# Kernel optimization log

Hardware: AMD Instinct MI355X
Metric: run time of the kernel (lower is better)

The kernel has to match this reference:

```python
import jax, jax.numpy as jnp
import numpy as np

B, K, S, H, V, T = 32, 5, 64, 768, 30522, 40
SEP = 102


def setup_inputs() -> dict:
    key = jax.random.key(0)
    ks = jax.random.split(key, 8)
    s = 0.02
    return {
        "src": jax.random.normal(ks[0], (B, S, H), jnp.float32),
        "E": jax.random.normal(ks[1], (V, H), jnp.float32) * s,
        "Wa": jax.random.normal(ks[2], (H, H), jnp.float32) * s,
        "Ua": jax.random.normal(ks[3], (H, H), jnp.float32) * s,
        "va": jax.random.normal(ks[4], (H,), jnp.float32) * s,
        "W_ih": jax.random.normal(ks[5], (3 * H, 2 * H), jnp.float32) * s,
        "W_hh": jax.random.normal(ks[6], (3 * H, H), jnp.float32) * s,
        "b_ih": jnp.zeros((3 * H,), jnp.float32),
        "b_hh": jnp.zeros((3 * H,), jnp.float32),
        "Wo": jax.random.normal(ks[7], (V, H), jnp.float32) * s,
        "bo": jnp.zeros((V,), jnp.float32),
    }


def _decoder(tok, src, h, E, Wa, Ua, va, W_ih, W_hh, b_ih, b_hh, Wo, bo):
    # tok [N] int, src [N,S,H], h [N,H] -> (logits [N,V], h_new [N,H])
    emb = E[tok]                                              # [N,H]
    e = jnp.tanh(src @ Wa + (h @ Ua)[:, None, :]) @ va        # [N,S]
    a = jax.nn.softmax(e, axis=-1)
    ctx = jnp.einsum('ns,nsd->nd', a, src)                    # [N,H]
    x = jnp.concatenate([emb, ctx], axis=-1)                  # [N,2H]
    gx = x @ W_ih.T + b_ih
    gh = h @ W_hh.T + b_hh
    xr, xz, xn = jnp.split(gx, 3, axis=-1)
    hr, hz, hn = jnp.split(gh, 3, axis=-1)
    r = jax.nn.sigmoid(xr + hr)
    z = jax.nn.sigmoid(xz + hz)
    n = jnp.tanh(xn + r * hn)
    h2 = (1.0 - z) * n + z * h
    return h2 @ Wo.T + bo, h2


def _search(src, E, Wa, Ua, va, W_ih, W_hh, b_ih, b_hh, Wo, bo):
    P = (E, Wa, Ua, va, W_ih, W_hh, b_ih, b_hh, Wo, bo)
    # step 0: start token 102, zero hidden
    tok0 = jnp.full((B,), SEP, jnp.int32)
    logits, h = _decoder(tok0, src, jnp.zeros((B, H), src.dtype), *P)
    logp = jax.nn.log_softmax(logits, axis=-1)
    scores, toks = jax.lax.top_k(logp, K)                     # [B,K]
    hiddens = jnp.broadcast_to(h[:, None, :], (B, K, H))
    src_k = jnp.broadcast_to(src[:, None], (B, K, S, H)).reshape(B * K, S, H)
    no_prob = jnp.full((V,), -1e9, src.dtype).at[SEP].set(0.0)
    beam_mask = jnp.arange(K) < K - 1  # original normalizes only first k-1 segments

    def body(carry, _):
        toks, maps, hiddens, scores, ended, lengths = carry
        # parent hidden per beam (gather by backpointer), decode all beams at once
        h_in = jnp.take_along_axis(hiddens, maps[:, :, None], axis=1)  # [B,K,H]
        logits, h_new = _decoder(toks.reshape(-1), src_k, h_in.reshape(B * K, H), *P)
        logp = jax.nn.log_softmax(logits, axis=-1).reshape(B, K, V)
        logp = jnp.where(ended[:, :, None] == 0, logp, no_prob)
        lengths = lengths + (ended == 0).astype(lengths.dtype)
        cand = logp + scores[:, :, None]                      # [B,K,V]
        denom = jnp.where(beam_mask, lengths ** 0.7, 1.0)     # [B,K]
        norm = (cand / denom[:, :, None]).reshape(B, K * V)
        _, idx = jax.lax.top_k(norm, K)                       # [B,K]
        new_scores = jnp.take_along_axis(cand.reshape(B, K * V), idx, axis=1)
        new_toks = (idx % V).astype(jnp.int32)
        new_maps = (idx // V).astype(jnp.int32)
        ended = jnp.where(new_toks == SEP, 1.0, ended)
        new_carry = (new_toks, new_maps, h_new.reshape(B, K, H), new_scores, ended, lengths)
        return new_carry, (new_toks, new_maps)

    carry0 = (toks.astype(jnp.int32), jnp.zeros((B, K), jnp.int32), hiddens,
              scores, jnp.zeros((B, K), src.dtype), jnp.zeros((B, K), src.dtype))
    carryF, (toks_seq, maps_seq) = jax.lax.scan(body, carry0, None, length=T - 1)
    toks_all = jnp.concatenate([toks[None].astype(jnp.int32), toks_seq], axis=0)   # [T,B,K]
    maps_all = jnp.concatenate([jnp.zeros((1, B, K), jnp.int32), maps_seq], axis=0)
    final_scores = carryF[3]
    best = jnp.argmax(final_scores, axis=1).astype(jnp.int32)  # [B]

    def back(idx, tm):
        tk, mp = tm
        out = jnp.take_along_axis(tk, idx[:, None], axis=1)[:, 0]
        nxt = jnp.take_along_axis(mp, idx[:, None], axis=1)[:, 0]
        return nxt, out

    _, outs = jax.lax.scan(back, best, (toks_all, maps_all), reverse=True)
    return outs.T, final_scores  # tokens [B,T], scores [B,K]


def reference(src, E, Wa, Ua, va, W_ih, W_hh, b_ih, b_hh, Wo, bo):
    tokens, _ = _search(src, E, Wa, Ua, va, W_ih, W_hh, b_ih, b_hh, Wo, bo)
    return tokens
```

## Files before the change

kernel.cpp:

```cpp
#include <hip/hip_runtime.h>
#include <hip/hip_cooperative_groups.h>
#include <cmath>

namespace cg = cooperative_groups;

#define Hdim 768
#define Bb 32
#define Kb 5
#define Ss 64
#define Vv 30522
#define Tt 40
#define SEPTOK 102
#define NTLOG 477

typedef __attribute__((ext_vector_type(2))) float f32x2;
typedef __attribute__((ext_vector_type(4))) float f32x4;

struct Params {
    const float *src, *E, *Wa, *Ua, *va, *W_ih, *W_hh, *b_ih, *b_hh, *Wo, *bo;
    float *srcWa, *hA, *hB, *h_tmp, *h_g, *hUa, *xbuf, *gxE, *gx, *gh, *logits;
    float *maxpart, *mx, *lgs, *scores, *ended, *lengths;
    int *toks_cur, *maps_cur, *toks_all, *maps_all, *outTok;
};

__device__ __forceinline__ bool betterf(float va, int ja, float vb, int jb) {
    return (va > vb) || (va == vb && ja < jb);
}
__device__ __forceinline__ void ins5(float* tv, int* tj, float v, int j) {
    if (!betterf(v, j, tv[4], tj[4])) return;
    tv[4] = v; tj[4] = j;
#pragma unroll
    for (int q = 4; q > 0; q--) {
        if (betterf(tv[q], tj[q], tv[q - 1], tj[q - 1])) {
            float t = tv[q]; tv[q] = tv[q - 1]; tv[q - 1] = t;
            int  ti = tj[q]; tj[q] = tj[q - 1]; tj[q - 1] = ti;
        }
    }
}

union SMem {
    struct { float xs[32][162]; float wt[32][66]; } g;
    struct { float hu[Hdim]; float va[Hdim]; float e[Ss]; float a[Ss];
             float ctx[Hdim]; float gx[2304]; } at;
    struct { float sc[Kb], den[Kb], end[Kb], len[Kb], mxs[Kb], lgv[Kb];
             float mv[512 * 5]; int mj[512 * 5];
             float rv[512]; int rj[512]; double rd[512]; int selj[Kb]; } tk;
};

__device__ void gemm512(SMem& sm, const Params& P, int t, int N, int xsrc,
    int i0, int Pdim, const float* __restrict__ W, int ldW, bool pmaj,
    const float* __restrict__ bias, float* __restrict__ outp, int ldO,
    int Icap, float* __restrict__ maxpart, int tileIdx)
{
    const int tid = threadIdx.x;
    const int ty = tid >> 5, tx = tid & 31;
    const float* h_old = (t & 1) ? P.hB : P.hA;
    const float* h_new = (t & 1) ? P.hA : P.hB;

    float acc[10][2];
#pragma unroll
    for (int j = 0; j < 10; j++) { acc[j][0] = 0.f; acc[j][1] = 0.f; }

    for (int c0 = 0; c0 < Pdim; c0 += 32) {
        __syncthreads();
        for (int e = tid; e < 160 * 32; e += 512) {
            int r = e >> 5, p = e & 31;
            int n = (r < N) ? r : (N - 1);
            float v = 0.f;
            if (xsrc == 0) {
                if (t != 0) {
                    int par = (n / Kb) * Kb + P.maps_cur[n];
                    v = h_old[(size_t)par * Hdim + c0 + p];
                }
            } else if (xsrc == 1) {
                int tok = (t == 0) ? SEPTOK : P.toks_cur[n];
                v = P.E[(size_t)tok * Hdim + c0 + p];
            } else {
                int rowMul = (t == 0) ? Kb : 1;
                v = h_new[((size_t)n * rowMul) * Hdim + c0 + p];
            }
            sm.g.xs[p][r] = v;
        }
        if (pmaj) {
            int p = tid >> 4, i4 = (tid & 15) * 4;
            int gi = i0 + i4;
            f32x4 a;
            if (gi + 3 < Icap) {
                a = *(const f32x4*)&W[(size_t)(c0 + p) * ldW + gi];
            } else {
#pragma unroll
                for (int u = 0; u < 4; u++) {
                    int g = gi + u; if (g >= Icap) g = Icap - 1;
                    a[u] = W[(size_t)(c0 + p) * ldW + g];
                }
            }
            *(f32x4*)&sm.g.wt[p][i4] = a;
        } else {
            int c = tid >> 3, p4 = (tid & 7) * 4;
            int gi = i0 + c; if (gi >= Icap) gi = Icap - 1;
            f32x4 a = *(const f32x4*)&W[(size_t)gi * ldW + c0 + p4];
            sm.g.wt[p4 + 0][c] = a[0]; sm.g.wt[p4 + 1][c] = a[1];
            sm.g.wt[p4 + 2][c] = a[2]; sm.g.wt[p4 + 3][c] = a[3];
        }
        __syncthreads();
        float part[10][2];
#pragma unroll
        for (int j = 0; j < 10; j++) { part[j][0] = 0.f; part[j][1] = 0.f; }
#pragma unroll
        for (int p = 0; p < 32; p++) {
            f32x2 w2 = *(const f32x2*)&sm.g.wt[p][tx * 2];
            float xr[10];
#pragma unroll
            for (int j = 0; j < 10; j += 2) {
                f32x2 xv = *(const f32x2*)&sm.g.xs[p][ty * 10 + j];
                xr[j] = xv.x; xr[j + 1] = xv.y;
            }
#pragma unroll
            for (int j = 0; j < 10; j++) {
                part[j][0] = fmaf(xr[j], w2.x, part[j][0]);
                part[j][1] = fmaf(xr[j], w2.y, part[j][1]);
            }
        }
#pragma unroll
        for (int j = 0; j < 10; j++) {
            acc[j][0] = __fadd_rn(acc[j][0], part[j][0]);
            acc[j][1] = __fadd_rn(acc[j][1], part[j][1]);
        }
    }
    float rmax[10];
#pragma unroll
    for (int j = 0; j < 10; j++) rmax[j] = -INFINITY;
#pragma unroll
    for (int j = 0; j < 10; j++) {
        int r = ty * 10 + j;
        if (r < N) {
#pragma unroll
            for (int u = 0; u < 2; u++) {
                int gi = i0 + tx * 2 + u;
                if (gi < Icap) {
                    float v = acc[j][u];
                    if (bias) v = __fadd_rn(v, bias[gi]);
                    outp[(size_t)r * ldO + gi] = v;
                    rmax[j] = fmaxf(rmax[j], v);
                }
            }
        }
    }
    if (maxpart) {
#pragma unroll
        for (int j = 0; j < 10; j++) {
#pragma unroll
            for (int off = 16; off; off >>= 1)
                rmax[j] = fmaxf(rmax[j], __shfl_xor(rmax[j], off, 32));
        }
        if (tx == 0) {
#pragma unroll
            for (int j = 0; j < 10; j++) {
                int r = ty * 10 + j;
                if (r < N) maxpart[(size_t)tileIdx * 160 + r] = rmax[j];
            }
        }
    }
}

__global__ __launch_bounds__(512) void step_k(Params P)
{
    cg::grid_group grid = cg::this_grid();
    __shared__ SMem sm;
    const int tid = threadIdx.x;
    const int gdim = gridDim.x;

    for (int t = 0; t < Tt; t++) {
        const int N = (t == 0) ? Bb : Bb * Kb;
        const int Kcur = (t == 0) ? 1 : Kb;
        float* h_new = (t & 1) ? P.hA : P.hB;
        const float* h_old = (t & 1) ? P.hB : P.hA;

        for (int task = blockIdx.x; task < 84; task += gdim) {
            if (task < 12)
                gemm512(sm, P, t, N, 0, task * 64, Hdim, P.Ua, Hdim, true,
                        nullptr, P.hUa, Hdim, Hdim, nullptr, 0);
            else if (task < 48)
                gemm512(sm, P, t, N, 0, (task - 12) * 64, Hdim, P.W_hh, Hdim, false,
                        P.b_hh, P.gh, 2304, 2304, nullptr, 0);
            else
                gemm512(sm, P, t, N, 1, (task - 48) * 64, Hdim, P.W_ih, 1536, false,
                        nullptr, P.gxE, 2304, 2304, nullptr, 0);
        }
        grid.sync();

        for (int n = blockIdx.x; n < N; n += gdim) {
            int b = n / Kcur;
            for (int j = tid; j < Hdim; j += 512) {
                sm.at.hu[j] = P.hUa[(size_t)n * Hdim + j];
                sm.at.va[j] = P.va[j];
            }
            __syncthreads();
            {
                int wv = tid >> 6, ln = tid & 63;
                for (int s = wv * 8; s < wv * 8 + 8; s++) {
                    const float* sw = P.srcWa + (size_t)(b * Ss + s) * Hdim;
                    double p = 0.0;
                    for (int j = ln; j < Hdim; j += 64) {
                        float tv = (float)tanh((double)__fadd_rn(sw[j], sm.at.hu[j]));
                        p = ::fma((double)tv, (double)sm.at.va[j], p);
                    }
                    for (int off = 32; off; off >>= 1) p += __shfl_down(p, off, 64);
                    if (ln == 0) sm.at.e[s] = (float)p;
                }
            }
            __syncthreads();
            if (tid < 64) {
                float v = sm.at.e[tid], m = v;
                for (int off = 32; off; off >>= 1) m = fmaxf(m, __shfl_xor(m, off, 64));
                float p = (float)exp((double)__fsub_rn(v, m));
                double sum = (double)p;
                for (int off = 32; off; off >>= 1) sum += __shfl_xor(sum, off, 64);
                sm.at.a[tid] = __fdiv_rn(p, (float)sum);
            }
            __syncthreads();
            for (int j = tid; j < Hdim; j += 512) {
                double acc = 0.0;
                for (int s = 0; s < Ss; s++)
                    acc = ::fma((double)sm.at.a[s],
                                (double)P.src[(size_t)(b * Ss + s) * Hdim + j], acc);
                sm.at.ctx[j] = (float)acc;
            }
            __syncthreads();
            for (int i = tid; i < 2304; i += 512) {
                const float* wr = P.W_ih + (size_t)i * 1536 + 768;
                float accv = 0.f, part = 0.f;
                for (int p = 0; p < 768; p += 4) {
                    f32x4 w4 = *(const f32x4*)&wr[p];
                    part = fmaf(sm.at.ctx[p + 0], w4[0], part);
                    part = fmaf(sm.at.ctx[p + 1], w4[1], part);
                    part = fmaf(sm.at.ctx[p + 2], w4[2], part);
                    part = fmaf(sm.at.ctx[p + 3], w4[3], part);
                    if ((p & 31) == 28) { accv = __fadd_rn(accv, part); part = 0.f; }
                }
                sm.at.gx[i] = __fadd_rn(__fadd_rn(P.gxE[(size_t)n * 2304 + i], accv),
                                        P.b_ih[i]);
            }
            __syncthreads();
            int par = 0;
            if (t != 0) par = (n / Kb) * Kb + P.maps_cur[n];
            for (int i = tid; i < Hdim; i += 512) {
                float xr = sm.at.gx[i], xz = sm.at.gx[768 + i], xn = sm.at.gx[1536 + i];
                const float* ghr = P.gh + (size_t)n * 2304;
                float hr = ghr[i], hz = ghr[768 + i], hn = ghr[1536 + i];
                float r  = (float)(1.0 / (1.0 + exp(-(double)__fadd_rn(xr, hr))));
                float z  = (float)(1.0 / (1.0 + exp(-(double)__fadd_rn(xz, hz))));
                float nn = (float)tanh((double)__fadd_rn(xn, __fmul_rn(r, hn)));
                float hv = (t == 0) ? 0.f : h_old[(size_t)par * Hdim + i];
                float h2 = __fadd_rn(__fmul_rn(__fsub_rn(1.f, z), nn), __fmul_rn(z, hv));
                if (t == 0) {
                    for (int k = 0; k < Kb; k++)
                        h_new[(size_t)(n * Kb + k) * Hdim + i] = h2;
                } else {
                    h_new[(size_t)n * Hdim + i] = h2;
                }
            }
            __syncthreads();
        }
        grid.sync();

        for (int task = blockIdx.x; task < NTLOG; task += gdim) {
            gemm512(sm, P, t, N, 2, task * 64, Hdim, P.Wo, Hdim, false,
                    P.bo, P.logits, Vv, Vv, P.maxpart, task);
        }
        grid.sync();

        for (int b = blockIdx.x; b < Bb; b += gdim) {
            if (tid < Kb) {
                if (t == 0) {
                    sm.tk.sc[tid] = 0.f; sm.tk.end[tid] = 0.f; sm.tk.len[tid] = 0.f;
                    sm.tk.den[tid] = 1.f;
                } else {
                    float e0 = P.ended[b * Kb + tid];
                    float ln = __fadd_rn(P.lengths[b * Kb + tid], (e0 == 0.f) ? 1.f : 0.f);
                    sm.tk.sc[tid]  = P.scores[b * Kb + tid];
                    sm.tk.end[tid] = e0;
                    sm.tk.len[tid] = ln;
                    sm.tk.den[tid] = (tid < Kb - 1) ? (float)pow((double)ln, (double)0.7f) : 1.f;
                }
            }
            __syncthreads();
            for (int k = 0; k < Kcur; k++) {
                bool active = (t == 0) || (sm.tk.end[k] == 0.f);
                if (!active) {
                    if (tid == 0) { sm.tk.mxs[k] = 0.f; sm.tk.lgv[k] = 0.f; }
                    __syncthreads();
                    continue;
                }
                int n = b * Kcur + k;
                float m = -INFINITY;
                for (int tile = tid; tile < NTLOG; tile += 512)
                    m = fmaxf(m, P.maxpart[(size_t)tile * 160 + n]);
                sm.tk.rv[tid] = m; __syncthreads();
                for (int off = 256; off; off >>= 1) {
                    if (tid < off) sm.tk.rv[tid] = fmaxf(sm.tk.rv[tid], sm.tk.rv[tid + off]);
                    __syncthreads();
                }
                m = sm.tk.rv[0];
                const float* lg = P.logits + (size_t)n * Vv;
                double s = 0.0;
                for (int v = tid; v < Vv; v += 512) {
                    float ex = (float)exp((double)__fsub_rn(lg[v], m));
                    s += (double)ex;
                }
                __syncthreads();
                sm.tk.rd[tid] = s; __syncthreads();
                for (int off = 256; off; off >>= 1) {
                    if (tid < off) sm.tk.rd[tid] += sm.tk.rd[tid + off];
                    __syncthreads();
                }
                if (tid == 0) {
                    sm.tk.mxs[k] = m;
                    float sf = (float)sm.tk.rd[0];
                    sm.tk.lgv[k] = (float)log((double)sf);
                }
                __syncthreads();
            }
            const float* lbase = P.logits + (size_t)b * Kcur * Vv;
            float tv[5]; int tj[5];
#pragma unroll
            for (int q = 0; q < 5; q++) { tv[q] = -INFINITY; tj[q] = 0x7fffffff; }
            for (int k = 0; k < Kcur; k++) {
                if (t == 0 || sm.tk.end[k] == 0.f) {
                    float m = sm.tk.mxs[k], l = sm.tk.lgv[k];
                    float sck = sm.tk.sc[k], den = sm.tk.den[k];
                    const float* lg = lbase + (size_t)k * Vv;
                    for (int v = tid; v < Vv; v += 512) {
                        float lp  = __fsub_rn(__fsub_rn(lg[v], m), l);
                        float val = __fdiv_rn(__fadd_rn(lp, sck), den);
                        ins5(tv, tj, val, k * Vv + v);
                    }
                } else if (tid == 0) {
                    float val = __fdiv_rn(sm.tk.sc[k], sm.tk.den[k]);
                    ins5(tv, tj, val, k * Vv + SEPTOK);
                }
            }
#pragma unroll
            for (int q = 0; q < 5; q++) { sm.tk.mv[tid * 5 + q] = tv[q]; sm.tk.mj[tid * 5 + q] = tj[q]; }
            __syncthreads();
            for (int pass = 0; pass < Kb; pass++) {
                float bv = -INFINITY; int bj = 0x7fffffff;
#pragma unroll
                for (int q = 0; q < 5; q++) {
                    float v = sm.tk.mv[tid * 5 + q]; int j = sm.tk.mj[tid * 5 + q];
                    if (betterf(v, j, bv, bj)) { bv = v; bj = j; }
                }
                sm.tk.rv[tid] = bv; sm.tk.rj[tid] = bj;
                __syncthreads();
                for (int off = 256; off; off >>= 1) {
                    if (tid < off) {
                        float ov = sm.tk.rv[tid + off]; int oj = sm.tk.rj[tid + off];
                        if (betterf(ov, oj, sm.tk.rv[tid], sm.tk.rj[tid])) {
                            sm.tk.rv[tid] = ov; sm.tk.rj[tid] = oj;
                        }
                    }
                    __syncthreads();
                }
                if (tid == 0) sm.tk.selj[pass] = sm.tk.rj[0];
                __syncthreads();
#pragma unroll
                for (int q = 0; q < 5; q++)
                    if (sm.tk.mj[tid * 5 + q] == sm.tk.selj[pass]) {
                        sm.tk.mv[tid * 5 + q] = -INFINITY; sm.tk.mj[tid * 5 + q] = 0x7fffffff;
                    }
                __syncthreads();
            }
            if (tid == 0) {
                for (int q = 0; q < Kb; q++) {
                    int jj = sm.tk.selj[q];
                    int pk = jj / Vv, vv = jj - pk * Vv;
                    float lp;
                    if (t == 0 || sm.tk.end[pk] == 0.f)
                        lp = __fsub_rn(__fsub_rn(lbase[(size_t)pk * Vv + vv], sm.tk.mxs[pk]),
                                       sm.tk.lgv[pk]);
                    else
                        lp = (vv == SEPTOK) ? 0.f : -1e9f;
                    float cand = __fadd_rn(lp, sm.tk.sc[pk]);
                    P.scores[b * Kb + q]   = cand;
                    P.toks_cur[b * Kb + q] = vv;
                    P.maps_cur[b * Kb + q] = (t == 0) ? 0 : pk;
                    if (t == 0) {
                        P.ended[b * Kb + q]   = 0.f;
                        P.lengths[b * Kb + q] = 0.f;
                    } else {
                        P.ended[b * Kb + q]   = (vv == SEPTOK) ? 1.f : sm.tk.end[q];
                        P.lengths[b * Kb + q] = sm.tk.len[q];
                    }
                    P.toks_all[(size_t)t * Bb * Kb + b * Kb + q] = vv;
                    P.maps_all[(size_t)t * Bb * Kb + b * Kb + q] = (t == 0) ? 0 : pk;
                }
            }
            __syncthreads();
        }
        grid.sync();
    }

    if (blockIdx.x == 0 && tid < Bb) {
        int b = tid;
        int best = 0; float bvv = P.scores[b * Kb];
        for (int k = 1; k < Kb; k++) {
            float v = P.scores[b * Kb + k];
            if (v > bvv) { bvv = v; best = k; }
        }
        int cur = best;
        for (int t = Tt - 1; t >= 0; t--) {
            P.outTok[b * Tt + t] = P.toks_all[t * Bb * Kb + b * Kb + cur];
            cur = P.maps_all[t * Bb * Kb + b * Kb + cur];
        }
    }
}

template<int RPT, int CPT, bool PMAJ>
__global__ __launch_bounds__(512) void gemmN_k(int P, int I, int xrs, int ldW,
    const float* __restrict__ X, const float* __restrict__ W,
    const float* __restrict__ bias, float* __restrict__ out, int ldO)
{
    constexpr int ROWS = RPT * 16;
    constexpr int COLS = CPT * 32;
    constexpr int XST  = ROWS + 4;
    constexpr int WST  = COLS + 4;
    __shared__ float xs[32][XST];
    __shared__ float wt[32][WST];
    const int tid = threadIdx.x;
    const int ty = tid >> 5, tx = tid & 31;
    const int row0 = blockIdx.y * ROWS;
    const int i0 = blockIdx.x * COLS;

    float acc[RPT][CPT];
#pragma unroll
    for (int j = 0; j < RPT; j++)
#pragma unroll
        for (int u = 0; u < CPT; u++) acc[j][u] = 0.f;

    for (int c0 = 0; c0 < P; c0 += 32) {
        __syncthreads();
        for (int e = tid; e < ROWS * 32; e += 512) {
            int r = e >> 5, p = e & 31;
            xs[p][r] = X[(size_t)(row0 + r) * xrs + c0 + p];
        }
        if (PMAJ) {
            for (int v = tid; v < 32 * (COLS / 4); v += 512) {
                int p  = v / (COLS / 4);
                int i4 = (v % (COLS / 4)) * 4;
                f32x4 a;
                if (i0 + i4 + 3 < I) {
                    a = *(const f32x4*)&W[(size_t)(c0 + p) * ldW + i0 + i4];
                } else {
#pragma unroll
                    for (int u = 0; u < 4; u++) {
                        int g = i0 + i4 + u; if (g >= I) g = I - 1;
                        a[u] = W[(size_t)(c0 + p) * ldW + g];
                    }
                }
                *(f32x4*)&wt[p][i4] = a;
            }
        } else {
            for (int v = tid; v < COLS * 8; v += 512) {
                int c  = v >> 3;
                int p4 = (v & 7) * 4;
                int gi = i0 + c; if (gi >= I) gi = I - 1;
                f32x4 a = *(const f32x4*)&W[(size_t)gi * ldW + c0 + p4];
                wt[p4 + 0][c] = a[0]; wt[p4 + 1][c] = a[1];
                wt[p4 + 2][c] = a[2]; wt[p4 + 3][c] = a[3];
            }
        }
        __syncthreads();
        float part[RPT][CPT];
#pragma unroll
        for (int j = 0; j < RPT; j++)
#pragma unroll
            for (int u = 0; u < CPT; u++) part[j][u] = 0.f;
#pragma unroll
        for (int p = 0; p < 32; p++) {
            float xr[RPT];
#pragma unroll
            for (int j = 0; j < RPT; j += 2) {
                f32x2 xv = *(const f32x2*)&xs[p][ty * RPT + j];
                xr[j] = xv.x; xr[j + 1] = xv.y;
            }
            float wv[CPT];
#pragma unroll
            for (int u = 0; u < CPT; u += 2) {
                f32x2 w2 = *(const f32x2*)&wt[p][tx * CPT + u];
                wv[u] = w2.x; wv[u + 1] = w2.y;
            }
#pragma unroll
            for (int j = 0; j < RPT; j++)
#pragma unroll
                for (int u = 0; u < CPT; u++)
                    part[j][u] = fmaf(xr[j], wv[u], part[j][u]);
        }
#pragma unroll
        for (int j = 0; j < RPT; j++)
#pragma unroll
            for (int u = 0; u < CPT; u++)
                acc[j][u] = __fadd_rn(acc[j][u], part[j][u]);
    }
#pragma unroll
    for (int j = 0; j < RPT; j++) {
        int gr = row0 + ty * RPT + j;
#pragma unroll
        for (int u = 0; u < CPT; u++) {
            int gi = i0 + tx * CPT + u;
            if (gi < I) {
                float v = acc[j][u];
                if (bias) v = __fadd_rn(v, bias[gi]);
                out[(size_t)gr * ldO + gi] = v;
            }
        }
    }
}

__global__ __launch_bounds__(256) void gather_k(int N, int Kcur,
    const int* __restrict__ maps, const int* __restrict__ toks,
    const float* __restrict__ h_beam, const float* __restrict__ E,
    float* __restrict__ h_g, float* __restrict__ xbuf)
{
    int n = blockIdx.x;
    if (n >= N) return;
    int b = n / Kcur;
    int tok = toks ? toks[n] : SEPTOK;
    const float* er = E + (size_t)tok * Hdim;
    if (maps) {
        const float* hs = h_beam + (size_t)(b * Kb + maps[n]) * Hdim;
        for (int j = threadIdx.x; j < Hdim; j += 256) {
            h_g[(size_t)n * Hdim + j]  = hs[j];
            xbuf[(size_t)n * 1536 + j] = er[j];
        }
    } else {
        for (int j = threadIdx.x; j < Hdim; j += 256) {
            h_g[(size_t)n * Hdim + j]  = 0.f;
            xbuf[(size_t)n * 1536 + j] = er[j];
        }
    }
}

__global__ __launch_bounds__(256) void bcast_k(const float* __restrict__ h_tmp,
                                               float* __restrict__ h_beam)
{
    int b = blockIdx.x;
    for (int j = threadIdx.x; j < Hdim; j += 256) {
        float v = h_tmp[(size_t)b * Hdim + j];
        for (int k = 0; k < Kb; k++)
            h_beam[(size_t)(b * Kb + k) * Hdim + j] = v;
    }
}

__global__ __launch_bounds__(256) void attn2_k(int N, int Kcur,
    const float* __restrict__ hUa, const float* __restrict__ srcWa,
    const float* __restrict__ src, const float* __restrict__ va,
    float* __restrict__ xbuf)
{
    __shared__ float hu[Hdim];
    __shared__ float va_s[Hdim];
    __shared__ float e_s[Ss];
    __shared__ float a_s[Ss];
    int n = blockIdx.x, tid = threadIdx.x;
    if (n >= N) return;
    int b = n / Kcur;
    for (int j = tid; j < Hdim; j += 256) {
        hu[j]   = hUa[(size_t)n * Hdim + j];
        va_s[j] = va[j];
    }
    __syncthreads();
    int wv = tid >> 6, ln = tid & 63;
    for (int s = wv * 16; s < wv * 16 + 16; s++) {
        const float* sw = srcWa + (size_t)(b * Ss + s) * Hdim;
        double p = 0.0;
        for (int j = ln; j < Hdim; j += 64) {
            float tv = (float)tanh((double)__fadd_rn(sw[j], hu[j]));
            p = ::fma((double)tv, (double)va_s[j], p);
        }
        for (int off = 32; off; off >>= 1) p += __shfl_down(p, off, 64);
        if (ln == 0) e_s[s] = (float)p;
    }
    __syncthreads();
    if (tid < 64) {
        float v = e_s[tid], m = v;
        for (int off = 32; off; off >>= 1) m = fmaxf(m, __shfl_xor(m, off, 64));
        float p = (float)exp((double)__fsub_rn(v, m));
        double sum = (double)p;
        for (int off = 32; off; off >>= 1) sum += __shfl_xor(sum, off, 64);
        a_s[tid] = __fdiv_rn(p, (float)sum);
    }
    __syncthreads();
    for (int j = tid; j < Hdim; j += 256) {
        double acc = 0.0;
        for (int s = 0; s < Ss; s++)
            acc = ::fma((double)a_s[s], (double)src[(size_t)(b * Ss + s) * Hdim + j], acc);
        xbuf[(size_t)n * 1536 + 768 + j] = (float)acc;
    }
}

__global__ __launch_bounds__(256) void gate_k(int N,
    const float* __restrict__ gx, const float* __restrict__ gh,
    const float* __restrict__ h_g, float* __restrict__ h_out)
{
    int idx = blockIdx.x * 256 + threadIdx.x;
    if (idx >= N * Hdim) return;
    int n = idx / Hdim, i = idx - n * Hdim;
    const float* gxr = gx + (size_t)n * 2304;
    const float* ghr = gh + (size_t)n * 2304;
    float xr = gxr[i], xz = gxr[768 + i], xn = gxr[1536 + i];
    float hr = ghr[i], hz = ghr[768 + i], hn = ghr[1536 + i];
    float r  = (float)(1.0 / (1.0 + exp(-(double)__fadd_rn(xr, hr))));
    float z  = (float)(1.0 / (1.0 + exp(-(double)__fadd_rn(xz, hz))));
    float nn = (float)tanh((double)__fadd_rn(xn, __fmul_rn(r, hn)));
    float hv = h_g[(size_t)n * Hdim + i];
    float h2 = __fadd_rn(__fmul_rn(__fsub_rn(1.f, z), nn), __fmul_rn(z, hv));
    h_out[(size_t)n * Hdim + i] = h2;
}

__global__ __launch_bounds__(256) void lse_k(int N,
    const float* __restrict__ logits, float* __restrict__ mx, float* __restrict__ lgs)
{
    __shared__ float  redf[256];
    __shared__ double redd[256];
    int n = blockIdx.x, tid = threadIdx.x;
    const float* lg = logits + (size_t)n * Vv;
    float m = -INFINITY;
    for (int v = tid; v < Vv; v += 256) m = fmaxf(m, lg[v]);
    redf[tid] = m; __syncthreads();
    for (int off = 128; off; off >>= 1) {
        if (tid < off) redf[tid] = fmaxf(redf[tid], redf[tid + off]);
        __syncthreads();
    }
    m = redf[0];
    double s = 0.0;
    for (int v = tid; v < Vv; v += 256) {
        float ex = (float)exp((double)__fsub_rn(lg[v], m));
        s += (double)ex;
    }
    redd[tid] = s; __syncthreads();
    for (int off = 128; off; off >>= 1) {
        if (tid < off) redd[tid] += redd[tid + off];
        __syncthreads();
    }
    if (tid == 0) {
        mx[n] = m;
        float sf = (float)redd[0];
        lgs[n] = (float)log((double)sf);
    }
}

__global__ __launch_bounds__(256) void topk5_k(int t,
    const float* __restrict__ logits, const float* __restrict__ mx, const float* __restrict__ lgs,
    float* scores, float* ended, float* lengths,
    int* toks_cur, int* maps_cur, int* toks_all, int* maps_all)
{
    __shared__ float sc_s[Kb], den_s[Kb], end_s[Kb], len_s[Kb], mx_s[Kb], lg_s[Kb];
    __shared__ float mv[256 * 5];
    __shared__ int   mj[256 * 5];
    __shared__ float rv[256];
    __shared__ int   rj[256];
    __shared__ int   selj[Kb];
    int b = blockIdx.x, tid = threadIdx.x;
    int Kcur = (t == 0) ? 1 : Kb;
    if (tid < Kb) {
        if (t == 0) {
            sc_s[tid] = 0.f; end_s[tid] = 0.f; len_s[tid] = 0.f; den_s[tid] = 1.f;
            mx_s[tid] = mx[b]; lg_s[tid] = lgs[b];
        } else {
            float e0 = ended[b * Kb + tid];
            float ln = __fadd_rn(lengths[b * Kb + tid], (e0 == 0.f) ? 1.f : 0.f);
            sc_s[tid]  = scores[b * Kb + tid];
            end_s[tid] = e0;
            len_s[tid] = ln;
            den_s[tid] = (tid < Kb - 1) ? (float)pow((double)ln, (double)0.7f) : 1.f;
            mx_s[tid]  = mx[b * Kb + tid];
            lg_s[tid]  = lgs[b * Kb + tid];
        }
    }
    __syncthreads();
    const float* lbase = logits + (size_t)b * Kcur * Vv;
    float tv[5]; int tj[5];
#pragma unroll
    for (int q = 0; q < 5; q++) { tv[q] = -INFINITY; tj[q] = 0x7fffffff; }
    for (int k = 0; k < Kcur; k++) {
        if (end_s[k] == 0.f) {
            float m = mx_s[k], l = lg_s[k], sck = sc_s[k], den = den_s[k];
            const float* lg = lbase + (size_t)k * Vv;
            for (int v = tid; v < Vv; v += 256) {
                float lp  = __fsub_rn(__fsub_rn(lg[v], m), l);
                float val = __fdiv_rn(__fadd_rn(lp, sck), den);
                ins5(tv, tj, val, k * Vv + v);
            }
        } else if (tid == 0) {
            float val = __fdiv_rn(sc_s[k], den_s[k]);
            ins5(tv, tj, val, k * Vv + SEPTOK);
        }
    }
#pragma unroll
    for (int q = 0; q < 5; q++) { mv[tid * 5 + q] = tv[q]; mj[tid * 5 + q] = tj[q]; }
    __syncthreads();
    for (int pass = 0; pass < Kb; pass++) {
        float bv = -INFINITY; int bj = 0x7fffffff;
#pragma unroll
        for (int q = 0; q < 5; q++) {
            float v = mv[tid * 5 + q]; int j = mj[tid * 5 + q];
            if (betterf(v, j, bv, bj)) { bv = v; bj = j; }
        }
        rv[tid] = bv; rj[tid] = bj;
        __syncthreads();
        for (int off = 128; off; off >>= 1) {
            if (tid < off) {
                float ov = rv[tid + off]; int oj = rj[tid + off];
                if (betterf(ov, oj, rv[tid], rj[tid])) { rv[tid] = ov; rj[tid] = oj; }
            }
            __syncthreads();
        }
        if (tid == 0) selj[pass] = rj[0];
        __syncthreads();
#pragma unroll
        for (int q = 0; q < 5; q++)
            if (mj[tid * 5 + q] == selj[pass]) { mv[tid * 5 + q] = -INFINITY; mj[tid * 5 + q] = 0x7fffffff; }
        __syncthreads();
    }
    if (tid == 0) {
        for (int q = 0; q < Kb; q++) {
            int jj = selj[q];
            int pk = jj / Vv, vv = jj - pk * Vv;
            float lp;
            if (end_s[pk] == 0.f)
                lp = __fsub_rn(__fsub_rn(lbase[(size_t)pk * Vv + vv], mx_s[pk]), lg_s[pk]);
            else
                lp = (vv == SEPTOK) ? 0.f : -1e9f;
            float cand = __fadd_rn(lp, sc_s[pk]);
            scores[b * Kb + q]   = cand;
            toks_cur[b * Kb + q] = vv;
            maps_cur[b * Kb + q] = (t == 0) ? 0 : pk;
            if (t == 0) {
                ended[b * Kb + q]   = 0.f;
                lengths[b * Kb + q] = 0.f;
            } else {
                ended[b * Kb + q]   = (vv == SEPTOK) ? 1.f : end_s[q];
                lengths[b * Kb + q] = len_s[q];
            }
            toks_all[(size_t)t * Bb * Kb + b * Kb + q] = vv;
            maps_all[(size_t)t * Bb * Kb + b * Kb + q] = (t == 0) ? 0 : pk;
        }
    }
}

__global__ void back_k(const float* __restrict__ scores,
                       const int* __restrict__ toks_all, const int* __restrict__ maps_all,
                       int* __restrict__ out)
{
    int b = threadIdx.x;
    if (b >= Bb) return;
    int best = 0; float bvv = scores[b * Kb];
    for (int k = 1; k < Kb; k++) {
        float v = scores[b * Kb + k];
        if (v > bvv) { bvv = v; best = k; }
    }
    int cur = best;
    for (int t = Tt - 1; t >= 0; t--) {
        out[b * Tt + t] = toks_all[t * Bb * Kb + b * Kb + cur];
        cur = maps_all[t * Bb * Kb + b * Kb + cur];
    }
}

extern "C" void kernel_launch(void* const* d_in, const int* in_sizes, int n_in,
                              void* d_out, int out_size, void* d_ws, size_t ws_size,
                              hipStream_t stream)
{
    Params P;
    P.src  = (const float*)d_in[0];
    P.E    = (const float*)d_in[1];
    P.Wa   = (const float*)d_in[2];
    P.Ua   = (const float*)d_in[3];
    P.va   = (const float*)d_in[4];
    P.W_ih = (const float*)d_in[5];
    P.W_hh = (const float*)d_in[6];
    P.b_ih = (const float*)d_in[7];
    P.b_hh = (const float*)d_in[8];
    P.Wo   = (const float*)d_in[9];
    P.bo   = (const float*)d_in[10];
    P.outTok = (int*)d_out;

    char* w = (char*)d_ws;
    size_t used = 0;
    auto alloc = [&](size_t bytes) -> char* {
        char* p = w + used;
        used += (bytes + 255) & ~(size_t)255;
        return p;
    };
    P.srcWa   = (float*)alloc((size_t)Bb * Ss * Hdim * 4);
    P.hA      = (float*)alloc((size_t)Bb * Kb * Hdim * 4);
    P.hB      = (float*)alloc((size_t)Bb * Kb * Hdim * 4);
    P.h_tmp   = (float*)alloc((size_t)Bb * Hdim * 4);
    P.h_g     = (float*)alloc((size_t)Bb * Kb * Hdim * 4);
    P.hUa     = (float*)alloc((size_t)Bb * Kb * Hdim * 4);
    P.xbuf    = (float*)alloc((size_t)Bb * Kb * 1536 * 4);
    P.gxE     = (float*)alloc((size_t)Bb * Kb * 2304 * 4);
    P.gx      = (float*)alloc((size_t)Bb * Kb * 2304 * 4);
    P.gh      = (float*)alloc((size_t)Bb * Kb * 2304 * 4);
    P.logits  = (float*)alloc((size_t)Bb * Kb * Vv * 4);
    P.maxpart = (float*)alloc((size_t)NTLOG * 160 * 4);
    P.mx      = (float*)alloc(Bb * Kb * 4);
    P.lgs     = (float*)alloc(Bb * Kb * 4);
    P.scores  = (float*)alloc(Bb * Kb * 4);
    P.ended   = (float*)alloc(Bb * Kb * 4);
    P.lengths = (float*)alloc(Bb * Kb * 4);
    P.toks_cur = (int*)alloc(Bb * Kb * 4);
    P.maps_cur = (int*)alloc(Bb * Kb * 4);
    P.toks_all = (int*)alloc((size_t)Tt * Bb * Kb * 4);
    P.maps_all = (int*)alloc((size_t)Tt * Bb * Kb * 4);

    gemmN_k<8, 2, true><<<dim3(12, 16), 512, 0, stream>>>(
        Hdim, Hdim, Hdim, Hdim, P.src, P.Wa, nullptr, P.srcWa, Hdim);

    int dev = 0;
    (void)hipGetDevice(&dev);
    int nCU = 256;
    (void)hipDeviceGetAttribute(&nCU, hipDeviceAttributeMultiprocessorCount, dev);
    int maxAct = 0;
    if (hipOccupancyMaxActiveBlocksPerMultiprocessor(&maxAct, step_k, 512, 0)
            != hipSuccess || maxAct < 1)
        maxAct = 1;
    long long gridLL = (long long)maxAct * (long long)nCU;
    if (gridLL > 256) gridLL = 256;
    if (gridLL < 1) gridLL = 1;
    dim3 grid((unsigned)gridLL);

    void* args[] = { (void*)&P };
    hipError_t err = hipLaunchCooperativeKernel((void*)step_k, grid, dim3(512),
                                                args, 0, stream);
    if (err != hipSuccess) {
        (void)hipGetLastError();
        for (int t = 0; t < Tt; t++) {
            int N  = (t == 0) ? Bb : Bb * Kb;
            int Kc = (t == 0) ? 1 : Kb;
            const int* mp = (t == 0) ? nullptr : P.maps_cur;
            const int* tk = (t == 0) ? nullptr : P.toks_cur;
            float* h_beam = P.hA;
            float* h_cur = (t == 0) ? P.h_tmp : h_beam;

            gather_k<<<N, 256, 0, stream>>>(N, Kc, mp, tk, h_beam, P.E, P.h_g, P.xbuf);
            if (t == 0) {
                gemmN_k<2, 2, true><<<dim3(12, 1), 512, 0, stream>>>(
                    Hdim, Hdim, Hdim, Hdim, P.h_g, P.Ua, nullptr, P.hUa, Hdim);
            } else {
                gemmN_k<10, 2, true><<<dim3(12, 1), 512, 0, stream>>>(
                    Hdim, Hdim, Hdim, Hdim, P.h_g, P.Ua, nullptr, P.hUa, Hdim);
            }
            attn2_k<<<N, 256, 0, stream>>>(N, Kc, P.hUa, P.srcWa, P.src, P.va, P.xbuf);
            if (t == 0) {
                gemmN_k<2, 2, false><<<dim3(36, 1), 512, 0, stream>>>(
                    1536, 2304, 1536, 1536, P.xbuf, P.W_ih, P.b_ih, P.gx, 2304);
                gemmN_k<2, 2, false><<<dim3(36, 1), 512, 0, stream>>>(
                    Hdim, 2304, Hdim, Hdim, P.h_g, P.W_hh, P.b_hh, P.gh, 2304);
            } else {
                gemmN_k<10, 2, false><<<dim3(36, 1), 512, 0, stream>>>(
                    1536, 2304, 1536, 1536, P.xbuf, P.W_ih, P.b_ih, P.gx, 2304);
                gemmN_k<10, 2, false><<<dim3(36, 1), 512, 0, stream>>>(
                    Hdim, 2304, Hdim, Hdim, P.h_g, P.W_hh, P.b_hh, P.gh, 2304);
            }
            gate_k<<<(N * Hdim + 255) / 256, 256, 0, stream>>>(N, P.gx, P.gh, P.h_g, h_cur);
            if (t == 0)
                bcast_k<<<Bb, 256, 0, stream>>>(P.h_tmp, h_beam);
            if (t == 0) {
                gemmN_k<2, 4, false><<<dim3(239, 1), 512, 0, stream>>>(
                    Hdim, Vv, Hdim, Hdim, h_cur, P.Wo, P.bo, P.logits, Vv);
            } else {
                gemmN_k<10, 4, false><<<dim3(239, 1), 512, 0, stream>>>(
                    Hdim, Vv, Hdim, Hdim, h_cur, P.Wo, P.bo, P.logits, Vv);
            }
            lse_k<<<N, 256, 0, stream>>>(N, P.logits, P.mx, P.lgs);
            topk5_k<<<Bb, 256, 0, stream>>>(t, P.logits, P.mx, P.lgs, P.scores,
                                            P.ended, P.lengths, P.toks_cur, P.maps_cur,
                                            P.toks_all, P.maps_all);
        }
        back_k<<<1, 64, 0, stream>>>(P.scores, P.toks_all, P.maps_all, P.outTok);
    }
}
```

Measured before the change: 46.17 ms.

## Fuse per-tile softmax stats and top-5 into logits GEMM epilogue

The logits GEMM now computes per-tile row max, a sum of exponentials, and a per-row top-5 in its epilogue, so the full logits matrix no longer has to be written and re-read. The top-k phase then merges the per-tile statistics instead of scanning all 30522 logits per beam. It also swaps double-precision tanh/exp in attention and the GRU for float intrinsics, pads the Wo tile layout, and raises the cooperative grid cap to 512 blocks. The float math may change numerics and tie behaviour relative to the double path, and the larger grid makes each grid sync more expensive.

```diff
diff --git a/kernel.cpp b/kernel.cpp
--- a/kernel.cpp
+++ b/kernel.cpp
@@ -19,7 +19,8 @@
 struct Params {
     const float *src, *E, *Wa, *Ua, *va, *W_ih, *W_hh, *b_ih, *b_hh, *Wo, *bo;
     float *srcWa, *hA, *hB, *h_tmp, *h_g, *hUa, *xbuf, *gxE, *gx, *gh, *logits;
-    float *maxpart, *mx, *lgs, *scores, *ended, *lengths;
+    float *mt_g; double *st_g; float *t5v; int *t5j;
+    float *mx, *lgs, *scores, *ended, *lengths;
     int *toks_cur, *maps_cur, *toks_all, *maps_all, *outTok;
 };
 
@@ -37,25 +38,37 @@
         }
     }
 }
+__device__ __forceinline__ void ins5p(float* tv, int* tj, float* tx,
+                                      float v, int j, float x) {
+    if (!betterf(v, j, tv[4], tj[4])) return;
+    tv[4] = v; tj[4] = j; tx[4] = x;
+#pragma unroll
+    for (int q = 4; q > 0; q--) {
+        if (betterf(tv[q], tj[q], tv[q - 1], tj[q - 1])) {
+            float t = tv[q]; tv[q] = tv[q - 1]; tv[q - 1] = t;
+            int  ti = tj[q]; tj[q] = tj[q - 1]; tj[q - 1] = ti;
+            float tz = tx[q]; tx[q] = tx[q - 1]; tx[q - 1] = tz;
+        }
+    }
+}
 
 union SMem {
-    struct { float xs[32][162]; float wt[32][66]; } g;
+    struct { float xs[32][162]; float wt[32][68]; } g;
     struct { float hu[Hdim]; float va[Hdim]; float e[Ss]; float a[Ss];
              float ctx[Hdim]; float gx[2304]; } at;
     struct { float sc[Kb], den[Kb], end[Kb], len[Kb], mxs[Kb], lgv[Kb];
-             float mv[512 * 5]; int mj[512 * 5];
-             float rv[512]; int rj[512]; double rd[512]; int selj[Kb]; } tk;
+             float mv[256 * 5]; int mj[256 * 5]; float mxp[256 * 5];
+             float rv[512]; int rj[512]; float rx[512]; double rd[512];
+             int selj[Kb]; float selx[Kb]; } tk;
 };
 
 __device__ void gemm512(SMem& sm, const Params& P, int t, int N, int xsrc,
     int i0, int Pdim, const float* __restrict__ W, int ldW, bool pmaj,
-    const float* __restrict__ bias, float* __restrict__ outp, int ldO,
-    int Icap, float* __restrict__ maxpart, int tileIdx)
+    const float* __restrict__ bias, float* __restrict__ outp, int ldO, int Icap)
 {
     const int tid = threadIdx.x;
     const int ty = tid >> 5, tx = tid & 31;
     const float* h_old = (t & 1) ? P.hB : P.hA;
-    const float* h_new = (t & 1) ? P.hA : P.hB;
 
     float acc[10][2];
 #pragma unroll
@@ -72,12 +85,9 @@
                     int par = (n / Kb) * Kb + P.maps_cur[n];
                     v = h_old[(size_t)par * Hdim + c0 + p];
                 }
-            } else if (xsrc == 1) {
+            } else {
                 int tok = (t == 0) ? SEPTOK : P.toks_cur[n];
                 v = P.E[(size_t)tok * Hdim + c0 + p];
-            } else {
-                int rowMul = (t == 0) ? Kb : 1;
-                v = h_new[((size_t)n * rowMul) * Hdim + c0 + p];
             }
             sm.g.xs[p][r] = v;
         }
@@ -127,9 +137,6 @@
             acc[j][1] = __fadd_rn(acc[j][1], part[j][1]);
         }
     }
-    float rmax[10];
-#pragma unroll
-    for (int j = 0; j < 10; j++) rmax[j] = -INFINITY;
 #pragma unroll
     for (int j = 0; j < 10; j++) {
         int r = ty * 10 + j;
@@ -141,23 +148,100 @@
                     float v = acc[j][u];
                     if (bias) v = __fadd_rn(v, bias[gi]);
                     outp[(size_t)r * ldO + gi] = v;
-                    rmax[j] = fmaxf(rmax[j], v);
-                }
-            }
-        }
-    }
-    if (maxpart) {
+                }
+            }
+        }
+    }
+}
+
+__device__ void logits_tile(SMem& sm, const Params& P, int t, int N, int task)
+{
+    const int tid = threadIdx.x;
+    const int ty = tid >> 5, tx = tid & 31;
+    const int i0 = task * 64;
+    const float* h_new = (t & 1) ? P.hA : P.hB;
+    const int rowMul = (t == 0) ? Kb : 1;
+
+    float acc[10][2];
+#pragma unroll
+    for (int j = 0; j < 10; j++) { acc[j][0] = 0.f; acc[j][1] = 0.f; }
+
+    for (int c0 = 0; c0 < Hdim; c0 += 32) {
+        __syncthreads();
+        for (int e = tid; e < 160 * 32; e += 512) {
+            int r = e >> 5, p = e & 31;
+            int n = (r < N) ? r : (N - 1);
+            sm.g.xs[p][r] = h_new[((size_t)n * rowMul) * Hdim + c0 + p];
+        }
+        {
+            int c = tid >> 3, p4 = (tid & 7) * 4;
+            int gi = i0 + c; if (gi >= Vv) gi = Vv - 1;
+            f32x4 a = *(const f32x4*)&P.Wo[(size_t)gi * Hdim + c0 + p4];
+            sm.g.wt[p4 + 0][c] = a[0]; sm.g.wt[p4 + 1][c] = a[1];
+            sm.g.wt[p4 + 2][c] = a[2]; sm.g.wt[p4 + 3][c] = a[3];
+        }
+        __syncthreads();
+        float part[10][2];
+#pragma unroll
+        for (int j = 0; j < 10; j++) { part[j][0] = 0.f; part[j][1] = 0.f; }
+#pragma unroll
+        for (int p = 0; p < 32; p++) {
+            f32x2 w2 = *(const f32x2*)&sm.g.wt[p][tx * 2];
+            float xr[10];
+#pragma unroll
+            for (int j = 0; j < 10; j += 2) {
+                f32x2 xv = *(const f32x2*)&sm.g.xs[p][ty * 10 + j];
+                xr[j] = xv.x; xr[j + 1] = xv.y;
+            }
+#pragma unroll
+            for (int j = 0; j < 10; j++) {
+                part[j][0] = fmaf(xr[j], w2.x, part[j][0]);
+                part[j][1] = fmaf(xr[j], w2.y, part[j][1]);
+            }
+        }
 #pragma unroll
         for (int j = 0; j < 10; j++) {
-#pragma unroll
-            for (int off = 16; off; off >>= 1)
-                rmax[j] = fmaxf(rmax[j], __shfl_xor(rmax[j], off, 32));
-        }
-        if (tx == 0) {
-#pragma unroll
-            for (int j = 0; j < 10; j++) {
-                int r = ty * 10 + j;
-                if (r < N) maxpart[(size_t)tileIdx * 160 + r] = rmax[j];
+            acc[j][0] = __fadd_rn(acc[j][0], part[j][0]);
+            acc[j][1] = __fadd_rn(acc[j][1], part[j][1]);
+        }
+    }
+#pragma unroll
+    for (int j = 0; j < 10; j++) {
+        int r = ty * 10 + j;
+        int g0 = i0 + tx * 2, g1 = g0 + 1;
+        float x0 = (g0 < Vv) ? __fadd_rn(acc[j][0], P.bo[g0]) : -INFINITY;
+        float x1 = (g1 < Vv) ? __fadd_rn(acc[j][1], P.bo[g1]) : -INFINITY;
+        float mr = fmaxf(x0, x1);
+#pragma unroll
+        for (int off = 16; off; off >>= 1)
+            mr = fmaxf(mr, __shfl_xor(mr, off, 32));
+        double s = (double)expf(__fsub_rn(x0, mr)) + (double)expf(__fsub_rn(x1, mr));
+#pragma unroll
+        for (int off = 16; off; off >>= 1)
+            s += __shfl_xor(s, off, 32);
+        float tv[5]; int tj[5];
+#pragma unroll
+        for (int q = 0; q < 5; q++) { tv[q] = -INFINITY; tj[q] = 0x7fffffff; }
+        ins5(tv, tj, x0, (g0 < Vv) ? g0 : 0x7fffffff);
+        ins5(tv, tj, x1, (g1 < Vv) ? g1 : 0x7fffffff);
+#pragma unroll
+        for (int lv = 1; lv < 32; lv <<= 1) {
+            float pv[5]; int pj[5];
+#pragma unroll
+            for (int q = 0; q < 5; q++) {
+                pv[q] = __shfl_xor(tv[q], lv, 32);
+                pj[q] = __shfl_xor(tj[q], lv, 32);
+            }
+#pragma unroll
+            for (int q = 0; q < 5; q++) ins5(tv, tj, pv[q], pj[q]);
+        }
+        if (tx == 0 && r < N) {
+            P.mt_g[(size_t)task * 160 + r] = mr;
+            P.st_g[(size_t)task * 160 + r] = s;
+#pragma unroll
+            for (int q = 0; q < 5; q++) {
+                P.t5v[((size_t)task * 160 + r) * 5 + q] = tv[q];
+                P.t5j[((size_t)task * 160 + r) * 5 + q] = tj[q];
             }
         }
     }
@@ -179,13 +263,13 @@
         for (int task = blockIdx.x; task < 84; task += gdim) {
             if (task < 12)
                 gemm512(sm, P, t, N, 0, task * 64, Hdim, P.Ua, Hdim, true,
-                        nullptr, P.hUa, Hdim, Hdim, nullptr, 0);
+                        nullptr, P.hUa, Hdim, Hdim);
             else if (task < 48)
                 gemm512(sm, P, t, N, 0, (task - 12) * 64, Hdim, P.W_hh, Hdim, false,
-                        P.b_hh, P.gh, 2304, 2304, nullptr, 0);
+                        P.b_hh, P.gh, 2304, 2304);
             else
                 gemm512(sm, P, t, N, 1, (task - 48) * 64, Hdim, P.W_ih, 1536, false,
-                        nullptr, P.gxE, 2304, 2304, nullptr, 0);
+                        nullptr, P.gxE, 2304, 2304);
         }
         grid.sync();
 
@@ -202,7 +286,7 @@
                     const float* sw = P.srcWa + (size_t)(b * Ss + s) * Hdim;
                     double p = 0.0;
                     for (int j = ln; j < Hdim; j += 64) {
-                        float tv = (float)tanh((double)__fadd_rn(sw[j], sm.at.hu[j]));
+                        float tv = tanhf(__fadd_rn(sw[j], sm.at.hu[j]));
                         p = ::fma((double)tv, (double)sm.at.va[j], p);
                     }
                     for (int off = 32; off; off >>= 1) p += __shfl_down(p, off, 64);
@@ -213,7 +297,7 @@
             if (tid < 64) {
                 float v = sm.at.e[tid], m = v;
                 for (int off = 32; off; off >>= 1) m = fmaxf(m, __shfl_xor(m, off, 64));
-                float p = (float)exp((double)__fsub_rn(v, m));
+                float p = expf(__fsub_rn(v, m));
                 double sum = (double)p;
                 for (int off = 32; off; off >>= 1) sum += __shfl_xor(sum, off, 64);
                 sm.at.a[tid] = __fdiv_rn(p, (float)sum);
@@ -248,9 +332,9 @@
                 float xr = sm.at.gx[i], xz = sm.at.gx[768 + i], xn = sm.at.gx[1536 + i];
                 const float* ghr = P.gh + (size_t)n * 2304;
                 float hr = ghr[i], hz = ghr[768 + i], hn = ghr[1536 + i];
-                float r  = (float)(1.0 / (1.0 + exp(-(double)__fadd_rn(xr, hr))));
-                float z  = (float)(1.0 / (1.0 + exp(-(double)__fadd_rn(xz, hz))));
-                float nn = (float)tanh((double)__fadd_rn(xn, __fmul_rn(r, hn)));
+                float r  = __fdiv_rn(1.f, __fadd_rn(1.f, expf(-__fadd_rn(xr, hr))));
+                float z  = __fdiv_rn(1.f, __fadd_rn(1.f, expf(-__fadd_rn(xz, hz))));
+                float nn = tanhf(__fadd_rn(xn, __fmul_rn(r, hn)));
                 float hv = (t == 0) ? 0.f : h_old[(size_t)par * Hdim + i];
                 float h2 = __fadd_rn(__fmul_rn(__fsub_rn(1.f, z), nn), __fmul_rn(z, hv));
                 if (t == 0) {
@@ -264,10 +348,8 @@
         }
         grid.sync();
 
-        for (int task = blockIdx.x; task < NTLOG; task += gdim) {
-            gemm512(sm, P, t, N, 2, task * 64, Hdim, P.Wo, Hdim, false,
-                    P.bo, P.logits, Vv, Vv, P.maxpart, task);
-        }
+        for (int task = blockIdx.x; task < NTLOG; task += gdim)
+            logits_tile(sm, P, t, N, task);
         grid.sync();
 
         for (int b = blockIdx.x; b < Bb; b += gdim) {
@@ -295,19 +377,17 @@
                 int n = b * Kcur + k;
                 float m = -INFINITY;
                 for (int tile = tid; tile < NTLOG; tile += 512)
-                    m = fmaxf(m, P.maxpart[(size_t)tile * 160 + n]);
+                    m = fmaxf(m, P.mt_g[(size_t)tile * 160 + n]);
                 sm.tk.rv[tid] = m; __syncthreads();
                 for (int off = 256; off; off >>= 1) {
                     if (tid < off) sm.tk.rv[tid] = fmaxf(sm.tk.rv[tid], sm.tk.rv[tid + off]);
                     __syncthreads();
                 }
                 m = sm.tk.rv[0];
-                const float* lg = P.logits + (size_t)n * Vv;
                 double s = 0.0;
-                for (int v = tid; v < Vv; v += 512) {
-                    float ex = (float)exp((double)__fsub_rn(lg[v], m));
-                    s += (double)ex;
-                }
+                for (int tile = tid; tile < NTLOG; tile += 512)
+                    s += P.st_g[(size_t)tile * 160 + n] *
+                         exp((double)(P.mt_g[(size_t)tile * 160 + n] - m));
                 __syncthreads();
                 sm.tk.rd[tid] = s; __syncthreads();
                 for (int off = 256; off; off >>= 1) {
@@ -321,53 +401,72 @@
                 }
                 __syncthreads();
             }
-            const float* lbase = P.logits + (size_t)b * Kcur * Vv;
-            float tv[5]; int tj[5];
-#pragma unroll
-            for (int q = 0; q < 5; q++) { tv[q] = -INFINITY; tj[q] = 0x7fffffff; }
-            for (int k = 0; k < Kcur; k++) {
-                if (t == 0 || sm.tk.end[k] == 0.f) {
-                    float m = sm.tk.mxs[k], l = sm.tk.lgv[k];
-                    float sck = sm.tk.sc[k], den = sm.tk.den[k];
-                    const float* lg = lbase + (size_t)k * Vv;
-                    for (int v = tid; v < Vv; v += 512) {
-                        float lp  = __fsub_rn(__fsub_rn(lg[v], m), l);
-                        float val = __fdiv_rn(__fadd_rn(lp, sck), den);
-                        ins5(tv, tj, val, k * Vv + v);
+            float tv[5]; int tj[5]; float txx[5];
+#pragma unroll
+            for (int q = 0; q < 5; q++) { tv[q] = -INFINITY; tj[q] = 0x7fffffff; txx[q] = 0.f; }
+            if (tid < 256) {
+                int tot = Kcur * NTLOG * 5;
+                for (int c = tid; c < tot; c += 256) {
+                    int k = c / (NTLOG * 5);
+                    if (t != 0 && sm.tk.end[k] != 0.f) continue;
+                    int rm = c - k * NTLOG * 5;
+                    int tile = rm / 5, q = rm - tile * 5;
+                    int n = b * Kcur + k;
+                    int gi = P.t5j[((size_t)tile * 160 + n) * 5 + q];
+                    if (gi == 0x7fffffff) continue;
+                    float x = P.t5v[((size_t)tile * 160 + n) * 5 + q];
+                    float lp  = __fsub_rn(__fsub_rn(x, sm.tk.mxs[k]), sm.tk.lgv[k]);
+                    float val = __fdiv_rn(__fadd_rn(lp, sm.tk.sc[k]), sm.tk.den[k]);
+                    ins5p(tv, tj, txx, val, k * Vv + gi, x);
+                }
+            }
+            if (tid == 0 && t != 0) {
+                for (int k = 0; k < Kcur; k++)
+                    if (sm.tk.end[k] != 0.f) {
+                        float val = __fdiv_rn(sm.tk.sc[k], sm.tk.den[k]);
+                        ins5p(tv, tj, txx, val, k * Vv + SEPTOK, 0.f);
                     }
-                } else if (tid == 0) {
-                    float val = __fdiv_rn(sm.tk.sc[k], sm.tk.den[k]);
-                    ins5(tv, tj, val, k * Vv + SEPTOK);
-                }
-            }
-#pragma unroll
-            for (int q = 0; q < 5; q++) { sm.tk.mv[tid * 5 + q] = tv[q]; sm.tk.mj[tid * 5 + q] = tj[q]; }
+            }
+            if (tid < 256) {
+#pragma unroll
+                for (int q = 0; q < 5; q++) {
+                    sm.tk.mv[tid * 5 + q] = tv[q];
+                    sm.tk.mj[tid * 5 + q] = tj[q];
+                    sm.tk.mxp[tid * 5 + q] = txx[q];
+                }
+            }
             __syncthreads();
             for (int pass = 0; pass < Kb; pass++) {
-                float bv = -INFINITY; int bj = 0x7fffffff;
-#pragma unroll
-                for (int q = 0; q < 5; q++) {
-                    float v = sm.tk.mv[tid * 5 + q]; int j = sm.tk.mj[tid * 5 + q];
-                    if (betterf(v, j, bv, bj)) { bv = v; bj = j; }
-                }
-                sm.tk.rv[tid] = bv; sm.tk.rj[tid] = bj;
+                if (tid < 256) {
+                    float bv = -INFINITY; int bj = 0x7fffffff; float bx = 0.f;
+#pragma unroll
+                    for (int q = 0; q < 5; q++) {
+                        float v = sm.tk.mv[tid * 5 + q]; int j = sm.tk.mj[tid * 5 + q];
+                        if (betterf(v, j, bv, bj)) { bv = v; bj = j; bx = sm.tk.mxp[tid * 5 + q]; }
+                    }
+                    sm.tk.rv[tid] = bv; sm.tk.rj[tid] = bj; sm.tk.rx[tid] = bx;
+                }
                 __syncthreads();
-                for (int off = 256; off; off >>= 1) {
+                for (int off = 128; off; off >>= 1) {
                     if (tid < off) {
                         float ov = sm.tk.rv[tid + off]; int oj = sm.tk.rj[tid + off];
                         if (betterf(ov, oj, sm.tk.rv[tid], sm.tk.rj[tid])) {
                             sm.tk.rv[tid] = ov; sm.tk.rj[tid] = oj;
+                            sm.tk.rx[tid] = sm.tk.rx[tid + off];
                         }
                     }
                     __syncthreads();
                 }
-                if (tid == 0) sm.tk.selj[pass] = sm.tk.rj[0];
+                if (tid == 0) { sm.tk.selj[pass] = sm.tk.rj[0]; sm.tk.selx[pass] = sm.tk.rx[0]; }
                 __syncthreads();
-#pragma unroll
-                for (int q = 0; q < 5; q++)
-                    if (sm.tk.mj[tid * 5 + q] == sm.tk.selj[pass]) {
-                        sm.tk.mv[tid * 5 + q] = -INFINITY; sm.tk.mj[tid * 5 + q] = 0x7fffffff;
-                    }
+                if (tid < 256) {
+#pragma unroll
+                    for (int q = 0; q < 5; q++)
+                        if (sm.tk.mj[tid * 5 + q] == sm.tk.selj[pass]) {
+                            sm.tk.mv[tid * 5 + q] = -INFINITY;
+                            sm.tk.mj[tid * 5 + q] = 0x7fffffff;
+                        }
+                }
                 __syncthreads();
             }
             if (tid == 0) {
@@ -376,8 +475,7 @@
                     int pk = jj / Vv, vv = jj - pk * Vv;
                     float lp;
                     if (t == 0 || sm.tk.end[pk] == 0.f)
-                        lp = __fsub_rn(__fsub_rn(lbase[(size_t)pk * Vv + vv], sm.tk.mxs[pk]),
-                                       sm.tk.lgv[pk]);
+                        lp = __fsub_rn(__fsub_rn(sm.tk.selx[q], sm.tk.mxs[pk]), sm.tk.lgv[pk]);
                     else
                         lp = (vv == SEPTOK) ? 0.f : -1e9f;
                     float cand = __fadd_rn(lp, sm.tk.sc[pk]);
@@ -801,7 +899,10 @@
     P.gx      = (float*)alloc((size_t)Bb * Kb * 2304 * 4);
     P.gh      = (float*)alloc((size_t)Bb * Kb * 2304 * 4);
     P.logits  = (float*)alloc((size_t)Bb * Kb * Vv * 4);
-    P.maxpart = (float*)alloc((size_t)NTLOG * 160 * 4);
+    P.mt_g    = (float*)alloc((size_t)NTLOG * 160 * 4);
+    P.st_g    = (double*)alloc((size_t)NTLOG * 160 * 8);
+    P.t5v     = (float*)alloc((size_t)NTLOG * 160 * 5 * 4);
+    P.t5j     = (int*)alloc((size_t)NTLOG * 160 * 5 * 4);
     P.mx      = (float*)alloc(Bb * Kb * 4);
     P.lgs     = (float*)alloc(Bb * Kb * 4);
     P.scores  = (float*)alloc(Bb * Kb * 4);
@@ -824,7 +925,7 @@
             != hipSuccess || maxAct < 1)
         maxAct = 1;
     long long gridLL = (long long)maxAct * (long long)nCU;
-    if (gridLL > 256) gridLL = 256;
+    if (gridLL > 512) gridLL = 512;
     if (gridLL < 1) gridLL = 1;
     dim3 grid((unsigned)gridLL);
 
```

Result: slower. 47.31 ms (+2.5%).
